# Performance work log

Hardware: AMD Instinct MI355X
Metric: run time of the kernel (lower is better)

The kernel has to match this reference:

```python
import jax, jax.numpy as jnp
import numpy as np


def _dsepconv(inp, vert, horiz, offx, offy, mask):
    # inp: [B,C,H,W]; vert/horiz: [B,F,H,W]; offx/offy/mask: [B,F*F,H,W]
    B, C, H, W = inp.shape
    F = vert.shape[1]
    FF = F * F
    dt = inp.dtype
    k = jnp.arange(FF)
    ki = (k // F).astype(dt)   # vertical tap index i
    kj = (k % F).astype(dt)    # horizontal tap index j
    half = jnp.asarray((F - 1) / 2.0, dt)
    ys = jnp.arange(H, dtype=dt)
    xs = jnp.arange(W, dtype=dt)
    # per-pixel deformable sample positions, [B,FF,H,W]
    py = offy + ys[None, None, :, None] + (ki - half)[None, :, None, None]
    px = offx + xs[None, None, None, :] + (kj - half)[None, :, None, None]
    py = jnp.clip(py, 0.0, H - 1)
    px = jnp.clip(px, 0.0, W - 1)
    y0f = jnp.floor(py)
    x0f = jnp.floor(px)
    wy = py - y0f   # bilinear fractional weights
    wx = px - x0f
    y0 = y0f.astype(jnp.int32)
    x0 = x0f.astype(jnp.int32)
    y1 = jnp.minimum(y0 + 1, H - 1)
    x1 = jnp.minimum(x0 + 1, W - 1)

    inp_flat = inp.reshape(B, C, H * W)

    def gather(yi, xi):
        # flat spatial gather per batch element -> [B,C,FF,H,W]
        idx = (yi * W + xi).reshape(B, FF * H * W)
        g = jax.vmap(lambda im, ix: im[:, ix])(inp_flat, idx)
        return g.reshape(B, C, FF, H, W)

    g00 = gather(y0, x0)
    g01 = gather(y0, x1)
    g10 = gather(y1, x0)
    g11 = gather(y1, x1)
    wy_ = wy[:, None]  # [B,1,FF,H,W]
    wx_ = wx[:, None]
    samp = (g00 * (1 - wy_) * (1 - wx_)
            + g01 * (1 - wy_) * wx_
            + g10 * wy_ * (1 - wx_)
            + g11 * wy_ * wx_)  # [B,C,FF,H,W]
    # separable mask-weighted tap weights: vert[i]*horiz[j]*mask[k]
    wtap = vert[:, k // F] * horiz[:, k % F] * mask  # [B,FF,H,W]
    return jnp.einsum('bkhw,bckhw->bchw', wtap, samp)


def setup_inputs() -> dict:
    key = jax.random.key(0)
    ks = jax.random.split(key, 6)
    B, C, H, W, F = 4, 3, 384, 384, 5
    return {
        'tensorInput': jax.random.normal(ks[0], (B, C, H, W), jnp.float32),
        'tensorVertical': jax.random.uniform(ks[1], (B, F, H, W), jnp.float32),
        'tensorHorizontal': jax.random.uniform(ks[2], (B, F, H, W), jnp.float32),
        'tensorOffsetX': jax.random.normal(ks[3], (B, F * F, H, W), jnp.float32),
        'tensorOffsetY': jax.random.normal(ks[4], (B, F * F, H, W), jnp.float32),
        'tensorMask': jax.random.uniform(ks[5], (B, F * F, H, W), jnp.float32),
    }


def reference(tensorInput, tensorVertical, tensorHorizontal, tensorOffsetX, tensorOffsetY, tensorMask):
    return _dsepconv(tensorInput, tensorVertical, tensorHorizontal,
                     tensorOffsetX, tensorOffsetY, tensorMask)
```

## Files before the change

### kernel.cpp

```cpp
#include <hip/hip_runtime.h>
#include <hip/hip_fp16.h>

#define BB 4
#define CC 3
#define HH 384
#define WW 384
#define FF 5
#define KK 25
#define HW (HH*WW)

#define TX 64
#define TY 8
#define MARG 8
#define RH (TY + 2*MARG + 1)
#define RW (TX + 2*MARG)
#define SMN (RH*RW)

typedef float fx2 __attribute__((ext_vector_type(2)));

__device__ __forceinline__ fx2 nt_load2(const float* p) {
    return __builtin_nontemporal_load((const fx2*)p);
}

__device__ __forceinline__ uint2 pack_px(float c0, float c1, float c2) {
    __half2 h01 = __floats2half2_rn(c0, c1);
    uint2 r;
    r.x = *(const unsigned int*)&h01;
    r.y = (unsigned int)__half_as_ushort(__float2half_rn(c2));
    return r;
}

__device__ __forceinline__ void unpack_px(uint2 r, float& c0, float& c1, float& c2) {
    float2 f01 = __half22float2(*(const __half2*)&r.x);
    c0 = f01.x; c1 = f01.y;
    c2 = __half2float(*(const __half*)&r.y);
}

__global__ __launch_bounds__(256) void dsepconv_kernel(
    const float* __restrict__ inp,
    const float* __restrict__ vert,
    const float* __restrict__ horiz,
    const float* __restrict__ offx,
    const float* __restrict__ offy,
    const float* __restrict__ mask,
    float* __restrict__ out)
{
    __shared__ uint2 smem[SMN];

    int tx = threadIdx.x & 31;
    int ty = threadIdx.x >> 5;
    int X  = blockIdx.x * TX;
    int Y  = blockIdx.y * TY;
    int xb = X + tx * 2;
    int y  = Y + ty;
    int b  = blockIdx.z;
    int ylo = Y - MARG, xlo = X - MARG;
    int planeoff = y * WW + xb;

    const float* c0p = inp + ((size_t)b * CC + 0) * HW;
    const float* c1p = inp + ((size_t)b * CC + 1) * HW;
    const float* c2p = inp + ((size_t)b * CC + 2) * HW;

    for (int p = threadIdx.x; p < SMN; p += 256) {
        int r = p / RW;
        int c = p - r * RW;
        int gy = min(max(ylo + r, 0), HH - 1);
        int gx = min(max(xlo + c, 0), WW - 1);
        int o  = gy * WW + gx;
        smem[p] = pack_px(c0p[o], c1p[o], c2p[o]);
    }
    __syncthreads();

    fx2 v2[FF], h2[FF];
#pragma unroll
    for (int f = 0; f < FF; ++f) {
        v2[f] = nt_load2(vert  + (b * FF + f) * HW + planeoff);
        h2[f] = nt_load2(horiz + (b * FF + f) * HW + planeoff);
    }

    float acc[2][3] = {{0.f,0.f,0.f},{0.f,0.f,0.f}};
    const float fy = (float)y;

    for (int ki = 0; ki < FF; ++ki) {
        float dy = fy + (float)(ki - 2);
        const float* ox_p = offx + (size_t)(b * KK + ki * FF) * HW + planeoff;
        const float* oy_p = offy + (size_t)(b * KK + ki * FF) * HW + planeoff;
        const float* m_p  = mask + (size_t)(b * KK + ki * FF) * HW + planeoff;
#pragma unroll
        for (int kj = 0; kj < FF; ++kj) {
            fx2 ox2 = nt_load2(ox_p + kj * HW);
            fx2 oy2 = nt_load2(oy_p + kj * HW);
            fx2 m2  = nt_load2(m_p  + kj * HW);
#pragma unroll
            for (int p = 0; p < 2; ++p) {
                float wt = v2[ki][p] * h2[kj][p] * m2[p];
                float py = oy2[p] + dy;
                float px = ox2[p] + (float)(xb + p + kj - 2);
                py = fminf(fmaxf(py, 0.f), (float)(HH - 1));
                px = fminf(fmaxf(px, 0.f), (float)(WW - 1));
                float y0f = floorf(py);
                float x0f = floorf(px);
                float wy = py - y0f;
                float wx = px - x0f;
                int y0 = (int)y0f;
                int x0 = (int)x0f;

                int y0r = y0 - ylo;
                int x0r = x0 - xlo;
                bool ok = ((unsigned)y0r <= (unsigned)(RH - 2)) &
                          ((unsigned)x0r <= (unsigned)(RW - 2));

                float s00c0,s00c1,s00c2, s01c0,s01c1,s01c2;
                float s10c0,s10c1,s10c2, s11c0,s11c1,s11c2;
                if (ok) {
                    int dxo = (x0 < WW - 1) ? 1 : 0;
                    int dyo = (y0 < HH - 1) ? RW : 0;
                    int a   = y0r * RW + x0r;
                    uint2 r00 = smem[a];
                    uint2 r01 = smem[a + dxo];
                    uint2 r10 = smem[a + dyo];
                    uint2 r11 = smem[a + dyo + dxo];
                    unpack_px(r00, s00c0, s00c1, s00c2);
                    unpack_px(r01, s01c0, s01c1, s01c2);
                    unpack_px(r10, s10c0, s10c1, s10c2);
                    unpack_px(r11, s11c0, s11c1, s11c2);
                } else {
                    int x1 = min(x0 + 1, WW - 1);
                    int y1 = min(y0 + 1, HH - 1);
                    int o00 = y0 * WW + x0, o01 = y0 * WW + x1;
                    int o10 = y1 * WW + x0, o11 = y1 * WW + x1;
                    s00c0 = c0p[o00]; s00c1 = c1p[o00]; s00c2 = c2p[o00];
                    s01c0 = c0p[o01]; s01c1 = c1p[o01]; s01c2 = c2p[o01];
                    s10c0 = c0p[o10]; s10c1 = c1p[o10]; s10c2 = c2p[o10];
                    s11c0 = c0p[o11]; s11c1 = c1p[o11]; s11c2 = c2p[o11];
                }

                float w00 = (1.f - wy) * (1.f - wx);
                float w01 = (1.f - wy) * wx;
                float w10 = wy * (1.f - wx);
                float w11 = wy * wx;

                acc[p][0] += wt * (s00c0*w00 + s01c0*w01 + s10c0*w10 + s11c0*w11);
                acc[p][1] += wt * (s00c1*w00 + s01c1*w01 + s10c1*w10 + s11c1*w11);
                acc[p][2] += wt * (s00c2*w00 + s01c2*w01 + s10c2*w10 + s11c2*w11);
            }
        }
    }

#pragma unroll
    for (int c = 0; c < CC; ++c) {
        fx2 o; o.x = acc[0][c]; o.y = acc[1][c];
        *(fx2*)(out + ((size_t)b * CC + c) * HW + planeoff) = o;
    }
}

extern "C" void kernel_launch(void* const* d_in, const int* in_sizes, int n_in,
                              void* d_out, int out_size, void* d_ws, size_t ws_size,
                              hipStream_t stream) {
    const float* inp   = (const float*)d_in[0];
    const float* vert  = (const float*)d_in[1];
    const float* horiz = (const float*)d_in[2];
    const float* offx  = (const float*)d_in[3];
    const float* offy  = (const float*)d_in[4];
    const float* mask  = (const float*)d_in[5];
    float* out = (float*)d_out;

    dim3 grid(WW / TX, HH / TY, BB);
    dsepconv_kernel<<<grid, 256, 0, stream>>>(
        inp, vert, horiz, offx, offy, mask, out);
}
```

Baseline: 254.8 us.

## Prepack input to half table, split LDS planes, branchless tile sampling

Adds a pre-pass kernel that packs the three input channels into a per-pixel half-precision table in workspace, so each block fills its tile with a single global read per pixel. The shared tile is now stored as separate 32-bit word rows per channel group, and its margins are widened. Bilinear taps are read from LDS unconditionally at clamped addresses, and the global-memory fallback runs only when some lane in the wave falls outside the tile. The aim is to cut tile-fill cost and branch divergence, at the price of an extra kernel launch and a full pass over the input.

```diff
diff --git a/kernel.cpp b/kernel.cpp
--- a/kernel.cpp
+++ b/kernel.cpp
@@ -11,10 +11,11 @@
 
 #define TX 64
 #define TY 8
-#define MARG 8
-#define RH (TY + 2*MARG + 1)
-#define RW (TX + 2*MARG)
-#define SMN (RH*RW)
+#define MX 10
+#define MY 9
+#define RH (TY + 2*MY + 2)
+#define RWS (TX + 2*MX + 2)
+#define SMN (RH*RWS)
 
 typedef float fx2 __attribute__((ext_vector_type(2)));
 
@@ -30,13 +31,18 @@
     return r;
 }
 
-__device__ __forceinline__ void unpack_px(uint2 r, float& c0, float& c1, float& c2) {
-    float2 f01 = __half22float2(*(const __half2*)&r.x);
-    c0 = f01.x; c1 = f01.y;
-    c2 = __half2float(*(const __half*)&r.y);
+__global__ __launch_bounds__(256) void pack_kernel(
+    const float* __restrict__ inp, uint2* __restrict__ tab)
+{
+    int t = blockIdx.x * blockDim.x + threadIdx.x;
+    if (t >= BB * HW) return;
+    int b = t / HW;
+    const float* p0 = inp + (size_t)t + (size_t)b * 2 * HW;
+    tab[t] = pack_px(p0[0], p0[HW], p0[2 * HW]);
 }
 
 __global__ __launch_bounds__(256) void dsepconv_kernel(
+    const uint2* __restrict__ tab,
     const float* __restrict__ inp,
     const float* __restrict__ vert,
     const float* __restrict__ horiz,
@@ -45,7 +51,7 @@
     const float* __restrict__ mask,
     float* __restrict__ out)
 {
-    __shared__ uint2 smem[SMN];
+    __shared__ unsigned int lds[RH * 2 * RWS];
 
     int tx = threadIdx.x & 31;
     int ty = threadIdx.x >> 5;
@@ -54,20 +60,18 @@
     int xb = X + tx * 2;
     int y  = Y + ty;
     int b  = blockIdx.z;
-    int ylo = Y - MARG, xlo = X - MARG;
+    int ylo = Y - MY, xlo = X - MX;
     int planeoff = y * WW + xb;
 
-    const float* c0p = inp + ((size_t)b * CC + 0) * HW;
-    const float* c1p = inp + ((size_t)b * CC + 1) * HW;
-    const float* c2p = inp + ((size_t)b * CC + 2) * HW;
-
+    const uint2* tb = tab + (size_t)b * HW;
     for (int p = threadIdx.x; p < SMN; p += 256) {
-        int r = p / RW;
-        int c = p - r * RW;
+        int r = p / RWS;
+        int c = p - r * RWS;
         int gy = min(max(ylo + r, 0), HH - 1);
         int gx = min(max(xlo + c, 0), WW - 1);
-        int o  = gy * WW + gx;
-        smem[p] = pack_px(c0p[o], c1p[o], c2p[o]);
+        uint2 q = tb[gy * WW + gx];
+        lds[(r * 2) * RWS + c]     = q.x;
+        lds[(r * 2 + 1) * RWS + c] = q.y;
     }
     __syncthreads();
 
@@ -77,6 +81,10 @@
         v2[f] = nt_load2(vert  + (b * FF + f) * HW + planeoff);
         h2[f] = nt_load2(horiz + (b * FF + f) * HW + planeoff);
     }
+
+    const float* c0p = inp + ((size_t)b * CC + 0) * HW;
+    const float* c1p = inp + ((size_t)b * CC + 1) * HW;
+    const float* c2p = inp + ((size_t)b * CC + 2) * HW;
 
     float acc[2][3] = {{0.f,0.f,0.f},{0.f,0.f,0.f}};
     const float fy = (float)y;
@@ -108,31 +116,40 @@
                 int y0r = y0 - ylo;
                 int x0r = x0 - xlo;
                 bool ok = ((unsigned)y0r <= (unsigned)(RH - 2)) &
-                          ((unsigned)x0r <= (unsigned)(RW - 2));
+                          ((unsigned)x0r <= (unsigned)(RWS - 2));
+                int yc = min(max(y0r, 0), RH - 2);
+                int xc = min(max(x0r, 0), RWS - 2);
+                int a0 = (yc * 2) * RWS + xc;
 
-                float s00c0,s00c1,s00c2, s01c0,s01c1,s01c2;
-                float s10c0,s10c1,s10c2, s11c0,s11c1,s11c2;
-                if (ok) {
-                    int dxo = (x0 < WW - 1) ? 1 : 0;
-                    int dyo = (y0 < HH - 1) ? RW : 0;
-                    int a   = y0r * RW + x0r;
-                    uint2 r00 = smem[a];
-                    uint2 r01 = smem[a + dxo];
-                    uint2 r10 = smem[a + dyo];
-                    uint2 r11 = smem[a + dyo + dxo];
-                    unpack_px(r00, s00c0, s00c1, s00c2);
-                    unpack_px(r01, s01c0, s01c1, s01c2);
-                    unpack_px(r10, s10c0, s10c1, s10c2);
-                    unpack_px(r11, s11c0, s11c1, s11c2);
-                } else {
-                    int x1 = min(x0 + 1, WW - 1);
-                    int y1 = min(y0 + 1, HH - 1);
-                    int o00 = y0 * WW + x0, o01 = y0 * WW + x1;
-                    int o10 = y1 * WW + x0, o11 = y1 * WW + x1;
-                    s00c0 = c0p[o00]; s00c1 = c1p[o00]; s00c2 = c2p[o00];
-                    s01c0 = c0p[o01]; s01c1 = c1p[o01]; s01c2 = c2p[o01];
-                    s10c0 = c0p[o10]; s10c1 = c1p[o10]; s10c2 = c2p[o10];
-                    s11c0 = c0p[o11]; s11c1 = c1p[o11]; s11c2 = c2p[o11];
+                unsigned p00 = lds[a0],           p01 = lds[a0 + 1];
+                unsigned q00 = lds[a0 + RWS],     q01 = lds[a0 + RWS + 1];
+                unsigned p10 = lds[a0 + 2*RWS],   p11 = lds[a0 + 2*RWS + 1];
+                unsigned q10 = lds[a0 + 3*RWS],   q11 = lds[a0 + 3*RWS + 1];
+
+                float2 f00 = __half22float2(*(const __half2*)&p00);
+                float2 f01 = __half22float2(*(const __half2*)&p01);
+                float2 f10 = __half22float2(*(const __half2*)&p10);
+                float2 f11 = __half22float2(*(const __half2*)&p11);
+                float s00c0 = f00.x, s00c1 = f00.y;
+                float s01c0 = f01.x, s01c1 = f01.y;
+                float s10c0 = f10.x, s10c1 = f10.y;
+                float s11c0 = f11.x, s11c1 = f11.y;
+                float s00c2 = __half2float(*(const __half*)&q00);
+                float s01c2 = __half2float(*(const __half*)&q01);
+                float s10c2 = __half2float(*(const __half*)&q10);
+                float s11c2 = __half2float(*(const __half*)&q11);
+
+                if (__builtin_expect(!__all((int)ok), 0)) {
+                    if (!ok) {
+                        int x1 = min(x0 + 1, WW - 1);
+                        int y1g = min(y0 + 1, HH - 1);
+                        int o00 = y0 * WW + x0,  o01 = y0 * WW + x1;
+                        int o10 = y1g * WW + x0, o11 = y1g * WW + x1;
+                        s00c0 = c0p[o00]; s00c1 = c1p[o00]; s00c2 = c2p[o00];
+                        s01c0 = c0p[o01]; s01c1 = c1p[o01]; s01c2 = c2p[o01];
+                        s10c0 = c0p[o10]; s10c1 = c1p[o10]; s10c2 = c2p[o10];
+                        s11c0 = c0p[o11]; s11c1 = c1p[o11]; s11c2 = c2p[o11];
+                    }
                 }
 
                 float w00 = (1.f - wy) * (1.f - wx);
@@ -164,8 +181,14 @@
     const float* offy  = (const float*)d_in[4];
     const float* mask  = (const float*)d_in[5];
     float* out = (float*)d_out;
+    uint2* tab = (uint2*)d_ws;
 
-    dim3 grid(WW / TX, HH / TY, BB);
-    dsepconv_kernel<<<grid, 256, 0, stream>>>(
-        inp, vert, horiz, offx, offy, mask, out);
+    {
+        pack_kernel<<<(BB * HW + 255) / 256, 256, 0, stream>>>(inp, tab);
+    }
+    {
+        dim3 grid(WW / TX, HH / TY, BB);
+        dsepconv_kernel<<<grid, 256, 0, stream>>>(
+            tab, inp, vert, horiz, offx, offy, mask, out);
+    }
 }
```

Result: no change. 250.3 us (-1.8%).
